# Kernel optimization log

Hardware: AMD Instinct MI355X
Metric: run time of the kernel (lower is better)

Reference implementation:

```python
import jax, jax.numpy as jnp
import numpy as np

N, E, B = 50000, 500000, 32
FEAT, HID, EDGE_DIM = 64, 128, 16
NUM_TASKS, TED, NCLS, TASKS_PER = 5000, 64, 3, 8
NLAYERS = 2


def setup_inputs() -> dict:
    key = jax.random.key(0)
    ks = jax.random.split(key, 20)
    s = 0.05
    inp = {
        "h": jax.random.normal(ks[0], (N, FEAT), jnp.float32),
        "x": jax.random.normal(ks[1], (N, 3), jnp.float32),
        "edge_index": jax.random.randint(ks[2], (2, E), 0, N, dtype=jnp.int32),
        "edge_attr": jax.random.normal(ks[3], (E, EDGE_DIM), jnp.float32),
        "batch": (jnp.arange(N, dtype=jnp.int32) * B // N).astype(jnp.int32),
        "tasks_indices": jnp.stack([
            jnp.repeat(jnp.arange(B, dtype=jnp.int32), TASKS_PER),
            jax.random.randint(ks[4], (B * TASKS_PER,), 0, NUM_TASKS, dtype=jnp.int32),
        ], axis=1),
        "batch_size": B,
        "embed_W": jax.random.normal(ks[5], (FEAT, HID), jnp.float32) * s,
        "embed_b": jnp.zeros((HID,), jnp.float32),
        "res_W": jax.random.normal(ks[6], (NLAYERS, HID, HID), jnp.float32) * s,
        "msg_W": jax.random.normal(ks[7], (NLAYERS, 2 * HID + 1, HID), jnp.float32) * s,
        "msg_b": jnp.zeros((NLAYERS, HID), jnp.float32),
        "upd_W": jax.random.normal(ks[8], (NLAYERS, 2 * HID, HID), jnp.float32) * s,
        "upd_b": jnp.zeros((NLAYERS, HID), jnp.float32),
        "mlp_W0": jax.random.normal(ks[9], (HID + TED, HID), jnp.float32) * s,
        "mlp_b0": jnp.zeros((HID,), jnp.float32),
        "mlp_W1": jax.random.normal(ks[10], (HID, HID), jnp.float32) * s,
        "mlp_b1": jnp.zeros((HID,), jnp.float32),
        "mlp_W2": jax.random.normal(ks[11], (HID, HID), jnp.float32) * s,
        "mlp_b2": jnp.zeros((HID,), jnp.float32),
        "mlp_W3": jax.random.normal(ks[12], (HID, NCLS), jnp.float32) * s,
        "mlp_b3": jnp.zeros((NCLS,), jnp.float32),
        "task_emb": jax.random.normal(ks[13], (NUM_TASKS, TED), jnp.float32),
    }
    return inp


def reference(h, x, edge_index, edge_attr, batch, tasks_indices, batch_size,
              embed_W, embed_b, res_W, msg_W, msg_b, upd_W, upd_b,
              mlp_W0, mlp_b0, mlp_W1, mlp_b1, mlp_W2, mlp_b2, mlp_W3, mlp_b3,
              task_emb):
    n = h.shape[0]
    row, col = edge_index[0], edge_index[1]
    # squared distances, identical across MP layers (positions never updated)
    dist = jnp.sum((x[row] - x[col]) ** 2, axis=1, keepdims=True)  # [E,1]
    emb = h @ embed_W + embed_b  # [N,HID]
    for l in range(NLAYERS):
        msg_in = jnp.concatenate([emb[row], emb[col], dist], axis=-1)  # [E,2H+1]
        msg = jax.nn.relu(msg_in @ msg_W[l] + msg_b[l])                # [E,H]
        aggr = jax.ops.segment_sum(msg, col, num_segments=n)           # [N,H]
        upd = jax.nn.relu(jnp.concatenate([emb, aggr], axis=-1) @ upd_W[l] + upd_b[l])
        emb = emb @ res_W[l] + upd
    # global mean pool per graph
    counts = jax.ops.segment_sum(jnp.ones((n,), emb.dtype), batch, num_segments=batch_size)
    pooled = jax.ops.segment_sum(emb, batch, num_segments=batch_size) / jnp.maximum(counts, 1.0)[:, None]
    # per-(protein, task) head; rows ordered as in the original dict-over-batch loop
    proto = tasks_indices[:, 0]
    tid = tasks_indices[:, 1]
    feat = jnp.concatenate([pooled[proto], task_emb[tid]], axis=-1)  # [K, H+TED]
    z = jax.nn.relu(feat @ mlp_W0 + mlp_b0)
    z = jax.nn.relu(z @ mlp_W1 + mlp_b1)
    z = jax.nn.relu(z @ mlp_W2 + mlp_b2)
    return z @ mlp_W3 + mlp_b3  # [K, NCLS]
```

## Files before the change

### kernel.cpp

```cpp
#include <hip/hip_runtime.h>

constexpr int NN = 50000;
constexpr int NE = 500000;
constexpr int NB = 32;
constexpr int NTROWS = 256;
constexpr int SCB = 196;
constexpr int NBLK64 = (NN + 63) / 64;

typedef __attribute__((ext_vector_type(8))) short bf16x8;
typedef __attribute__((ext_vector_type(4))) float f32x4;

static __device__ __forceinline__ unsigned short f2bf(float f) {
  unsigned u = __float_as_uint(f);
  unsigned r = (u + 0x7FFFu + ((u >> 16) & 1u)) >> 16;
  return (unsigned short)r;
}
static __device__ __forceinline__ float bf2f(unsigned short s) {
  return __uint_as_float(((unsigned)s) << 16);
}

__global__ void k_wprep(const float* __restrict__ msgW, const float* __restrict__ updW,
                        const float* __restrict__ resW, const float* __restrict__ embW,
                        unsigned short* __restrict__ wbf, int* __restrict__ cnt) {
  int idx = blockIdx.x * 256 + threadIdx.x;
  if (idx < NN) cnt[idx] = 0;
  if (idx >= 10 * 16384 + 8192) return;
  if (idx < 10 * 16384) {
    int m = idx >> 14, e = idx & 16383;
    int nn = e >> 7, kk = e & 127;
    int l = m / 5, t = m % 5;
    const float* src;
    if (t == 0)      src = msgW + (size_t)l * 257 * 128;
    else if (t == 1) src = msgW + (size_t)l * 257 * 128 + 128 * 128;
    else if (t == 2) src = updW + (size_t)l * 256 * 128;
    else if (t == 3) src = updW + (size_t)l * 256 * 128 + 128 * 128;
    else             src = resW + (size_t)l * 128 * 128;
    wbf[idx] = f2bf(src[kk * 128 + nn]);
  } else {
    int e = idx - 10 * 16384;
    int nn = e >> 6, kk = e & 63;
    wbf[idx] = f2bf(embW[kk * 128 + nn]);
  }
}

__global__ void k_count_gstart(const int* __restrict__ col, int* __restrict__ cnt,
                               const int* __restrict__ batch, int* __restrict__ gstart) {
  int e = blockIdx.x * 256 + threadIdx.x;
  if (e < NE) atomicAdd(&cnt[col[e]], 1);
  if (e < NN) {
    int b = batch[e];
    if (e == 0) gstart[b] = 0;
    else if (batch[e - 1] != b) gstart[b] = e;
    if (e == NN - 1) gstart[b + 1] = NN;
  }
}

__global__ __launch_bounds__(256) void k_scan1(const int* __restrict__ cnt,
                                               int* __restrict__ starts,
                                               int* __restrict__ bsum) {
  __shared__ int s[256];
  int t = threadIdx.x;
  int i = blockIdx.x * 256 + t;
  int v = (i < NN) ? cnt[i] : 0;
  s[t] = v; __syncthreads();
  for (int off = 1; off < 256; off <<= 1) {
    int u = (t >= off) ? s[t - off] : 0;
    __syncthreads();
    s[t] += u;
    __syncthreads();
  }
  if (i < NN) starts[i] = s[t] - v;
  if (t == 255) bsum[blockIdx.x] = s[255];
}

__global__ __launch_bounds__(256) void k_scan2(int* __restrict__ bsum) {
  __shared__ int s[256];
  int t = threadIdx.x;
  int v = (t < SCB) ? bsum[t] : 0;
  s[t] = v; __syncthreads();
  for (int off = 1; off < 256; off <<= 1) {
    int u = (t >= off) ? s[t - off] : 0;
    __syncthreads();
    s[t] += u;
    __syncthreads();
  }
  if (t < SCB) bsum[t] = s[t] - v;
}

__global__ __launch_bounds__(256) void k_scan3(int* __restrict__ starts,
                                               const int* __restrict__ bsum,
                                               int* __restrict__ cursor) {
  int i = blockIdx.x * 256 + threadIdx.x;
  if (i < NN) {
    int v = starts[i] + bsum[blockIdx.x];
    starts[i] = v;
    cursor[i] = v;
  }
  if (i == 0) starts[NN] = NE;
}

__global__ void k_scatter(const int* __restrict__ row, const int* __restrict__ col,
                          const float* __restrict__ x,
                          int* __restrict__ cursor, int2* __restrict__ spack) {
  int e = blockIdx.x * blockDim.x + threadIdx.x;
  if (e >= NE) return;
  int r = row[e], c = col[e];
  float dx = x[3*r+0] - x[3*c+0];
  float dy = x[3*r+1] - x[3*c+1];
  float dz = x[3*r+2] - x[3*c+2];
  float d = dx*dx + dy*dy + dz*dz;
  int pos = atomicAdd(&cursor[c], 1);
  spack[pos] = make_int2(r, __float_as_int(d));
}

template<int TPB>
static __device__ __forceinline__ void stage_tile64(
    unsigned short* lds, const unsigned short* __restrict__ src, int row0, int n, int tid) {
  #pragma unroll
  for (int ch = tid; ch < 1024; ch += TPB) {
    int r = ch >> 4, kc = ch & 15;
    bf16x8 v = {0,0,0,0,0,0,0,0};
    if (row0 + r < n) v = *(const bf16x8*)(src + (size_t)(row0 + r) * 128 + kc * 8);
    int byte = (r * 256 + kc * 16) ^ ((r & 7) << 4);
    *(bf16x8*)((char*)lds + byte) = v;
  }
}

template<int TPB>
static __device__ __forceinline__ void vstore_tile64(
    unsigned short* __restrict__ dst, const unsigned short* lds, int row0, int n, int tid) {
  #pragma unroll
  for (int ch = tid; ch < 1024; ch += TPB) {
    int r = ch >> 4, kc = ch & 15;
    if (row0 + r < n) {
      bf16x8 v = *(const bf16x8*)((const char*)lds + ((r * 256 + kc * 16) ^ ((r & 7) << 4)));
      *(bf16x8*)(dst + (size_t)(row0 + r) * 128 + kc * 8) = v;
    }
  }
}

static __device__ __forceinline__ void epi_to_lds64(
    unsigned short* lds, const f32x4 (&acc)[4], int lane, int c0) {
  int ccol = lane & 15, crow4 = (lane >> 4) * 4;
  int cc = c0 + ccol;
  #pragma unroll
  for (int rt = 0; rt < 4; ++rt)
    #pragma unroll
    for (int j = 0; j < 4; ++j) {
      int lrow = rt * 16 + crow4 + j;
      int lbyte = (lrow * 256 + cc * 2) ^ ((lrow & 7) << 4);
      *(unsigned short*)((char*)lds + lbyte) = f2bf(acc[rt][j]);
    }
}

__global__ __launch_bounds__(512) void k_embed_dual(
    const float* __restrict__ h, const unsigned short* __restrict__ embWt,
    const float* __restrict__ embB,
    const unsigned short* __restrict__ W1t, const unsigned short* __restrict__ W2t,
    unsigned short* __restrict__ emb, unsigned short* __restrict__ Y1,
    unsigned short* __restrict__ Y2, int n) {
  __shared__ unsigned short Hs[64 * 64];
  __shared__ unsigned short Xs[64 * 128];
  __shared__ unsigned short Y1s[64 * 128];
  __shared__ unsigned short Y2s[64 * 128];
  int row0 = blockIdx.x * 64;
  int tid = threadIdx.x;
  int wave = tid >> 6, lane = tid & 63;
  int c0 = wave * 16;
  int arow = lane & 15, kb = (lane >> 4) * 8;
  {
    int r = tid >> 3, kc = tid & 7;
    union { bf16x8 v; unsigned short s[8]; } u;
    if (row0 + r < n) {
      const float* p = h + (size_t)(row0 + r) * 64 + kc * 8;
      float4 f0 = *(const float4*)p, f1 = *(const float4*)(p + 4);
      u.s[0]=f2bf(f0.x); u.s[1]=f2bf(f0.y); u.s[2]=f2bf(f0.z); u.s[3]=f2bf(f0.w);
      u.s[4]=f2bf(f1.x); u.s[5]=f2bf(f1.y); u.s[6]=f2bf(f1.z); u.s[7]=f2bf(f1.w);
    } else {
      #pragma unroll
      for (int j = 0; j < 8; ++j) u.s[j] = 0;
    }
    int byte = (r * 128 + kc * 16) ^ ((r & 7) << 4);
    *(bf16x8*)((char*)Hs + byte) = u.v;
  }
  float bB = embB[c0 + (lane & 15)];
  __syncthreads();
  f32x4 accE[4] = {};
  #pragma unroll
  for (int ks = 0; ks < 2; ++ks) {
    bf16x8 b = *(const bf16x8*)(embWt + (size_t)(c0 + arow) * 64 + ks * 32 + kb);
    #pragma unroll
    for (int rt = 0; rt < 4; ++rt) {
      int r = rt * 16 + arow;
      int byte = (r * 128 + (ks * 32 + kb) * 2) ^ ((r & 7) << 4);
      bf16x8 a = *(const bf16x8*)((const char*)Hs + byte);
      accE[rt] = __builtin_amdgcn_mfma_f32_16x16x32_bf16(a, b, accE[rt], 0, 0, 0);
    }
  }
  {
    int ccol = lane & 15, crow4 = (lane >> 4) * 4;
    int cc = c0 + ccol;
    #pragma unroll
    for (int rt = 0; rt < 4; ++rt)
      #pragma unroll
      for (int j = 0; j < 4; ++j) {
        int lrow = rt * 16 + crow4 + j;
        int lbyte = (lrow * 256 + cc * 2) ^ ((lrow & 7) << 4);
        *(unsigned short*)((char*)Xs + lbyte) = f2bf(accE[rt][j] + bB);
      }
  }
  __syncthreads();
  f32x4 acc1[4] = {};
  f32x4 acc2[4] = {};
  #pragma unroll
  for (int ks = 0; ks < 4; ++ks) {
    int k0 = ks * 32;
    bf16x8 b1 = *(const bf16x8*)(W1t + (size_t)(c0 + arow) * 128 + k0 + kb);
    bf16x8 b2 = *(const bf16x8*)(W2t + (size_t)(c0 + arow) * 128 + k0 + kb);
    #pragma unroll
    for (int rt = 0; rt < 4; ++rt) {
      int r = rt * 16 + arow;
      int byte = (r * 256 + (k0 + kb) * 2) ^ ((r & 7) << 4);
      bf16x8 a = *(const bf16x8*)((const char*)Xs + byte);
      acc1[rt] = __builtin_amdgcn_mfma_f32_16x16x32_bf16(a, b1, acc1[rt], 0, 0, 0);
      acc2[rt] = __builtin_amdgcn_mfma_f32_16x16x32_bf16(a, b2, acc2[rt], 0, 0, 0);
    }
  }
  vstore_tile64<512>(emb, Xs, row0, n, tid);
  epi_to_lds64(Y1s, acc1, lane, c0);
  epi_to_lds64(Y2s, acc2, lane, c0);
  __syncthreads();
  vstore_tile64<512>(Y1, Y1s, row0, n, tid);
  vstore_tile64<512>(Y2, Y2s, row0, n, tid);
}

__global__ __launch_bounds__(512) void k_node_dual(
    const unsigned short* __restrict__ emb, const unsigned short* __restrict__ aggr,
    const unsigned short* __restrict__ U1t, const unsigned short* __restrict__ U2t,
    const unsigned short* __restrict__ Rt, const float* __restrict__ updb,
    const unsigned short* __restrict__ W1t, const unsigned short* __restrict__ W2t,
    unsigned short* __restrict__ out, unsigned short* __restrict__ Y1,
    unsigned short* __restrict__ Y2, int n) {
  __shared__ unsigned short Es[64 * 128];
  __shared__ unsigned short As[64 * 128];
  __shared__ unsigned short Xs[64 * 128];
  int row0 = blockIdx.x * 64;
  int tid = threadIdx.x;
  int wave = tid >> 6, lane = tid & 63;
  int c0 = wave * 16;
  int arow = lane & 15, kb = (lane >> 4) * 8;
  stage_tile64<512>(Es, emb,  row0, n, tid);
  stage_tile64<512>(As, aggr, row0, n, tid);
  float uB = updb[c0 + (lane & 15)];
  __syncthreads();
  f32x4 accU[4] = {};
  f32x4 accR[4] = {};
  #pragma unroll
  for (int ks = 0; ks < 4; ++ks) {
    int k0 = ks * 32;
    bf16x8 bU1 = *(const bf16x8*)(U1t + (size_t)(c0 + arow) * 128 + k0 + kb);
    bf16x8 bU2 = *(const bf16x8*)(U2t + (size_t)(c0 + arow) * 128 + k0 + kb);
    bf16x8 bR  = *(const bf16x8*)(Rt  + (size_t)(c0 + arow) * 128 + k0 + kb);
    #pragma unroll
    for (int rt = 0; rt < 4; ++rt) {
      int r = rt * 16 + arow;
      int byte = (r * 256 + (k0 + kb) * 2) ^ ((r & 7) << 4);
      bf16x8 aE = *(const bf16x8*)((const char*)Es + byte);
      bf16x8 aA = *(const bf16x8*)((const char*)As + byte);
      accU[rt] = __builtin_amdgcn_mfma_f32_16x16x32_bf16(aE, bU1, accU[rt], 0, 0, 0);
      accU[rt] = __builtin_amdgcn_mfma_f32_16x16x32_bf16(aA, bU2, accU[rt], 0, 0, 0);
      accR[rt] = __builtin_amdgcn_mfma_f32_16x16x32_bf16(aE, bR,  accR[rt], 0, 0, 0);
    }
  }
  {
    int ccol = lane & 15, crow4 = (lane >> 4) * 4;
    int cc = c0 + ccol;
    #pragma unroll
    for (int rt = 0; rt < 4; ++rt)
      #pragma unroll
      for (int j = 0; j < 4; ++j) {
        int lrow = rt * 16 + crow4 + j;
        int lbyte = (lrow * 256 + cc * 2) ^ ((lrow & 7) << 4);
        *(unsigned short*)((char*)Xs + lbyte) =
            f2bf(accR[rt][j] + fmaxf(accU[rt][j] + uB, 0.f));
      }
  }
  __syncthreads();
  f32x4 acc1[4] = {};
  f32x4 acc2[4] = {};
  #pragma unroll
  for (int ks = 0; ks < 4; ++ks) {
    int k0 = ks * 32;
    bf16x8 b1 = *(const bf16x8*)(W1t + (size_t)(c0 + arow) * 128 + k0 + kb);
    bf16x8 b2 = *(const bf16x8*)(W2t + (size_t)(c0 + arow) * 128 + k0 + kb);
    #pragma unroll
    for (int rt = 0; rt < 4; ++rt) {
      int r = rt * 16 + arow;
      int byte = (r * 256 + (k0 + kb) * 2) ^ ((r & 7) << 4);
      bf16x8 a = *(const bf16x8*)((const char*)Xs + byte);
      acc1[rt] = __builtin_amdgcn_mfma_f32_16x16x32_bf16(a, b1, acc1[rt], 0, 0, 0);
      acc2[rt] = __builtin_amdgcn_mfma_f32_16x16x32_bf16(a, b2, acc2[rt], 0, 0, 0);
    }
  }
  vstore_tile64<512>(out, Xs, row0, n, tid);
  epi_to_lds64(Es, acc1, lane, c0);
  epi_to_lds64(As, acc2, lane, c0);
  __syncthreads();
  vstore_tile64<512>(Y1, Es, row0, n, tid);
  vstore_tile64<512>(Y2, As, row0, n, tid);
}

__global__ __launch_bounds__(512) void k_node_pool(
    const unsigned short* __restrict__ emb, const unsigned short* __restrict__ aggr,
    const unsigned short* __restrict__ U1t, const unsigned short* __restrict__ U2t,
    const unsigned short* __restrict__ Rt, const float* __restrict__ updb,
    const int* __restrict__ batch,
    float* __restrict__ ppart, int* __restrict__ pgid, int n) {
  __shared__ unsigned short Es[64 * 128];
  __shared__ unsigned short As[64 * 128];
  __shared__ int sbat[64];
  int row0 = blockIdx.x * 64;
  int tid = threadIdx.x;
  int wave = tid >> 6, lane = tid & 63;
  int c0 = wave * 16;
  int arow = lane & 15, kb = (lane >> 4) * 8;
  stage_tile64<512>(Es, emb,  row0, n, tid);
  stage_tile64<512>(As, aggr, row0, n, tid);
  if (tid < 64) sbat[tid] = batch[min(row0 + tid, n - 1)];
  float uB = updb[c0 + (lane & 15)];
  __syncthreads();
  f32x4 accU[4] = {};
  f32x4 accR[4] = {};
  #pragma unroll
  for (int ks = 0; ks < 4; ++ks) {
    int k0 = ks * 32;
    bf16x8 bU1 = *(const bf16x8*)(U1t + (size_t)(c0 + arow) * 128 + k0 + kb);
    bf16x8 bU2 = *(const bf16x8*)(U2t + (size_t)(c0 + arow) * 128 + k0 + kb);
    bf16x8 bR  = *(const bf16x8*)(Rt  + (size_t)(c0 + arow) * 128 + k0 + kb);
    #pragma unroll
    for (int rt = 0; rt < 4; ++rt) {
      int r = rt * 16 + arow;
      int byte = (r * 256 + (k0 + kb) * 2) ^ ((r & 7) << 4);
      bf16x8 aE = *(const bf16x8*)((const char*)Es + byte);
      bf16x8 aA = *(const bf16x8*)((const char*)As + byte);
      accU[rt] = __builtin_amdgcn_mfma_f32_16x16x32_bf16(aE, bU1, accU[rt], 0, 0, 0);
      accU[rt] = __builtin_amdgcn_mfma_f32_16x16x32_bf16(aA, bU2, accU[rt], 0, 0, 0);
      accR[rt] = __builtin_amdgcn_mfma_f32_16x16x32_bf16(aE, bR,  accR[rt], 0, 0, 0);
    }
  }
  int g0 = sbat[0];
  int crow4 = (lane >> 4) * 4;
  float s0 = 0.f, s1 = 0.f;
  #pragma unroll
  for (int rt = 0; rt < 4; ++rt)
    #pragma unroll
    for (int j = 0; j < 4; ++j) {
      int lrow = rt * 16 + crow4 + j;
      if (row0 + lrow < n) {
        float v = accR[rt][j] + fmaxf(accU[rt][j] + uB, 0.f);
        if (sbat[lrow] == g0) s0 += v; else s1 += v;
      }
    }
  s0 += __shfl_xor(s0, 16); s0 += __shfl_xor(s0, 32);
  s1 += __shfl_xor(s1, 16); s1 += __shfl_xor(s1, 32);
  if ((lane >> 4) == 0) {
    int cc = c0 + (lane & 15);
    ppart[(size_t)(2 * blockIdx.x) * 128 + cc] = s0;
    ppart[(size_t)(2 * blockIdx.x + 1) * 128 + cc] = s1;
  }
  if (tid == 0) {
    int gl = sbat[63];
    pgid[2 * blockIdx.x] = g0;
    pgid[2 * blockIdx.x + 1] = (gl != g0) ? gl : -1;
  }
}

__global__ __launch_bounds__(256) void k_aggr_pull(
    const int* __restrict__ starts, const int2* __restrict__ spack,
    const unsigned short* __restrict__ A, const unsigned short* __restrict__ Bm,
    const float* __restrict__ wd, const float* __restrict__ mb,
    unsigned short* __restrict__ aggr) {
  int t = blockIdx.x * 256 + threadIdx.x;
  int node = t >> 4;
  if (node >= NN) return;
  int c0 = (t & 15) * 8;
  union { bf16x8 v; unsigned short s[8]; } ub;
  ub.v = *(const bf16x8*)(Bm + (size_t)node * 128 + c0);
  float4 w0 = *(const float4*)(wd + c0), w1 = *(const float4*)(wd + c0 + 4);
  float4 bb0 = *(const float4*)(mb + c0), bb1 = *(const float4*)(mb + c0 + 4);
  float wv[8]   = {w0.x, w0.y, w0.z, w0.w, w1.x, w1.y, w1.z, w1.w};
  float bv[8]   = {bb0.x, bb0.y, bb0.z, bb0.w, bb1.x, bb1.y, bb1.z, bb1.w};
  float basev[8], accv[8];
  #pragma unroll
  for (int j = 0; j < 8; ++j) { basev[j] = bf2f(ub.s[j]) + bv[j]; accv[j] = 0.f; }
  int s = starts[node], e = starts[node + 1];
  int i = s;
  for (; i + 4 <= e; i += 4) {
    int2 p0 = spack[i + 0], p1 = spack[i + 1];
    int2 p2 = spack[i + 2], p3 = spack[i + 3];
    union { bf16x8 v; unsigned short s[8]; } a0, a1, a2, a3;
    a0.v = *(const bf16x8*)(A + (size_t)p0.x * 128 + c0);
    a1.v = *(const bf16x8*)(A + (size_t)p1.x * 128 + c0);
    a2.v = *(const bf16x8*)(A + (size_t)p2.x * 128 + c0);
    a3.v = *(const bf16x8*)(A + (size_t)p3.x * 128 + c0);
    float d0 = __int_as_float(p0.y), d1 = __int_as_float(p1.y);
    float d2 = __int_as_float(p2.y), d3 = __int_as_float(p3.y);
    #pragma unroll
    for (int j = 0; j < 8; ++j) {
      accv[j] += fmaxf(bf2f(a0.s[j]) + fmaf(d0, wv[j], basev[j]), 0.f);
      accv[j] += fmaxf(bf2f(a1.s[j]) + fmaf(d1, wv[j], basev[j]), 0.f);
      accv[j] += fmaxf(bf2f(a2.s[j]) + fmaf(d2, wv[j], basev[j]), 0.f);
      accv[j] += fmaxf(bf2f(a3.s[j]) + fmaf(d3, wv[j], basev[j]), 0.f);
    }
  }
  for (; i < e; ++i) {
    int2 p = spack[i];
    union { bf16x8 v; unsigned short s[8]; } a;
    a.v = *(const bf16x8*)(A + (size_t)p.x * 128 + c0);
    float d = __int_as_float(p.y);
    #pragma unroll
    for (int j = 0; j < 8; ++j)
      accv[j] += fmaxf(bf2f(a.s[j]) + fmaf(d, wv[j], basev[j]), 0.f);
  }
  union { bf16x8 v; unsigned short s[8]; } o;
  #pragma unroll
  for (int j = 0; j < 8; ++j) o.s[j] = f2bf(accv[j]);
  *(bf16x8*)(aggr + (size_t)node * 128 + c0) = o.v;
}

__global__ __launch_bounds__(128) void k_pool2(const float* __restrict__ ppart,
                                               const int* __restrict__ pgid,
                                               const int* __restrict__ gstart,
                                               float* __restrict__ pooled) {
  int g = blockIdx.x, t = threadIdx.x;
  int blo = gstart[g] >> 6;
  int bhi = (gstart[g + 1] - 1) >> 6;
  float acc = 0.f;
  for (int b = blo; b <= bhi; ++b) {
    if (pgid[2 * b] == g)     acc += ppart[(size_t)(2 * b) * 128 + t];
    if (pgid[2 * b + 1] == g) acc += ppart[(size_t)(2 * b + 1) * 128 + t];
  }
  float cntf = (float)(gstart[g + 1] - gstart[g]);
  pooled[g * 128 + t] = acc / fmaxf(cntf, 1.f);
}

__global__ __launch_bounds__(128) void k_head(
    const float* __restrict__ pooled, const float* __restrict__ temb,
    const int* __restrict__ tasks,
    const float* __restrict__ W0, const float* __restrict__ b0,
    const float* __restrict__ W1, const float* __restrict__ b1,
    const float* __restrict__ W2, const float* __restrict__ b2,
    const float* __restrict__ W3, const float* __restrict__ b3,
    float* __restrict__ out) {
  __shared__ float f[192];
  __shared__ float za[128];
  __shared__ float zb[128];
  int rowi = blockIdx.x, t = threadIdx.x;
  int proto = tasks[rowi*2 + 0];
  int tid2  = tasks[rowi*2 + 1];
  f[t] = pooled[proto*128 + t];
  if (t < 64) f[128 + t] = temb[(size_t)tid2*64 + t];
  __syncthreads();
  float a = b0[t];
  for (int k = 0; k < 192; ++k) a += f[k] * W0[k*128 + t];
  za[t] = fmaxf(a, 0.f);
  __syncthreads();
  a = b1[t];
  for (int k = 0; k < 128; ++k) a += za[k] * W1[k*128 + t];
  zb[t] = fmaxf(a, 0.f);
  __syncthreads();
  a = b2[t];
  for (int k = 0; k < 128; ++k) a += zb[k] * W2[k*128 + t];
  za[t] = fmaxf(a, 0.f);
  __syncthreads();
  if (t < 3) {
    a = b3[t];
    for (int k = 0; k < 128; ++k) a += za[k] * W3[k*3 + t];
    out[rowi*3 + t] = a;
  }
}

extern "C" void kernel_launch(void* const* d_in, const int* in_sizes, int n_in,
                              void* d_out, int out_size, void* d_ws, size_t ws_size,
                              hipStream_t stream) {
  const float* h    = (const float*)d_in[0];
  const float* x    = (const float*)d_in[1];
  const int*   ei   = (const int*)d_in[2];
  const int*   batch= (const int*)d_in[4];
  const int*   tasks= (const int*)d_in[5];
  const float* embW = (const float*)d_in[7];
  const float* embB = (const float*)d_in[8];
  const float* resW = (const float*)d_in[9];
  const float* msgW = (const float*)d_in[10];
  const float* msgB = (const float*)d_in[11];
  const float* updW = (const float*)d_in[12];
  const float* updB = (const float*)d_in[13];
  const float* W0 = (const float*)d_in[14]; const float* b0 = (const float*)d_in[15];
  const float* W1 = (const float*)d_in[16]; const float* b1 = (const float*)d_in[17];
  const float* W2 = (const float*)d_in[18]; const float* b2 = (const float*)d_in[19];
  const float* W3 = (const float*)d_in[20]; const float* b3 = (const float*)d_in[21];
  const float* temb = (const float*)d_in[22];
  const int* row = ei;
  const int* col = ei + NE;

  unsigned short* bws = (unsigned short*)d_ws;
  unsigned short* e0   = bws;  bws += (size_t)NN*128;
  unsigned short* e1   = bws;  bws += (size_t)NN*128;
  unsigned short* Abuf = bws;  bws += (size_t)NN*128;
  unsigned short* Bbuf = bws;  bws += (size_t)NN*128;
  unsigned short* wbf  = bws;  bws += 10*16384 + 8192;
  float* ws = (float*)bws;
  float* pooled= ws;  ws += NB*128;
  float* ppart = ws;  ws += (size_t)2*NBLK64*128;
  int2*  spack = (int2*)ws;
  int*   iws   = (int*)(spack + NE);
  int*   cnt    = iws;  iws += NN;
  int*   starts = iws;  iws += NN + 1;
  int*   cursor = iws;  iws += NN;
  int*   gstart = iws;  iws += NB + 1;
  int*   bsum   = iws;  iws += 256;
  int*   pgid   = iws;  iws += 2*NBLK64;

  const unsigned short* embWt = wbf + (size_t)10*16384;

  k_wprep<<<672, 256, 0, stream>>>(msgW, updW, resW, embW, wbf, cnt);

  k_count_gstart<<<(NE + 255)/256, 256, 0, stream>>>(col, cnt, batch, gstart);
  k_scan1<<<SCB, 256, 0, stream>>>(cnt, starts, bsum);
  k_scan2<<<1, 256, 0, stream>>>(bsum);
  k_scan3<<<SCB, 256, 0, stream>>>(starts, bsum, cursor);
  k_scatter<<<(NE + 255)/256, 256, 0, stream>>>(row, col, x, cursor, spack);

  const unsigned short* m0W1t = wbf + (size_t)0 * 16384;
  const unsigned short* m0W2t = wbf + (size_t)1 * 16384;
  const unsigned short* u0W1t = wbf + (size_t)2 * 16384;
  const unsigned short* u0W2t = wbf + (size_t)3 * 16384;
  const unsigned short* r0Wt  = wbf + (size_t)4 * 16384;
  const unsigned short* m1W1t = wbf + (size_t)5 * 16384;
  const unsigned short* m1W2t = wbf + (size_t)6 * 16384;
  const unsigned short* u1W1t = wbf + (size_t)7 * 16384;
  const unsigned short* u1W2t = wbf + (size_t)8 * 16384;
  const unsigned short* r1Wt  = wbf + (size_t)9 * 16384;

  k_embed_dual<<<NBLK64, 512, 0, stream>>>(h, embWt, embB, m0W1t, m0W2t,
                                           e0, Abuf, Bbuf, NN);
  k_aggr_pull<<<(NN*16 + 255)/256, 256, 0, stream>>>(starts, spack, Abuf, Bbuf,
                                                     msgW + 256*128, msgB, e1);
  k_node_dual<<<NBLK64, 512, 0, stream>>>(e0, e1, u0W1t, u0W2t, r0Wt, updB,
                                          m1W1t, m1W2t, e1, Abuf, Bbuf, NN);
  k_aggr_pull<<<(NN*16 + 255)/256, 256, 0, stream>>>(starts, spack, Abuf, Bbuf,
                                                     msgW + (size_t)257*128 + 256*128,
                                                     msgB + 128, e0);
  k_node_pool<<<NBLK64, 512, 0, stream>>>(e1, e0, u1W1t, u1W2t, r1Wt, updB + 128,
                                          batch, ppart, pgid, NN);
  k_pool2<<<NB, 128, 0, stream>>>(ppart, pgid, gstart, pooled);
  k_head<<<NTROWS, 128, 0, stream>>>(pooled, temb, tasks,
                                     W0, b0, W1, b1, W2, b2, W3, b3, (float*)d_out);
}
```

Before: 213.6 us.

## Fuse edge-message pull aggregation into node update kernels via LDS staging

The separate k_aggr_pull kernels are removed. Each node-update block now gathers and aggregates the incoming-edge messages for its own 64 nodes straight into shared memory before the MFMA update. This saves two launches and the write and read-back of the aggregate buffer. Because the next layer's A/B buffers are written while other blocks still read the current ones, A/B are double-buffered, which adds workspace. The trade-off is that the gather now runs inside 512-thread, LDS-heavy blocks with fewer nodes in flight, which may hide the irregular gather latency less well than the standalone kernel did.

```diff
diff --git a/kernel.cpp b/kernel.cpp
--- a/kernel.cpp
+++ b/kernel.cpp
@@ -151,6 +151,67 @@
       int lbyte = (lrow * 256 + cc * 2) ^ ((lrow & 7) << 4);
       *(unsigned short*)((char*)lds + lbyte) = f2bf(acc[rt][j]);
     }
+}
+
+static __device__ __forceinline__ void gather_aggr_lds(
+    unsigned short* As, const int* __restrict__ starts, const int2* __restrict__ spack,
+    const unsigned short* __restrict__ A, const unsigned short* __restrict__ Bm,
+    const float* __restrict__ wd, const float* __restrict__ mb,
+    int row0, int n, int tid) {
+  int c0 = (tid & 15) * 8;
+  float4 w0 = *(const float4*)(wd + c0), w1 = *(const float4*)(wd + c0 + 4);
+  float4 bb0 = *(const float4*)(mb + c0), bb1 = *(const float4*)(mb + c0 + 4);
+  float wv[8] = {w0.x, w0.y, w0.z, w0.w, w1.x, w1.y, w1.z, w1.w};
+  float bv[8] = {bb0.x, bb0.y, bb0.z, bb0.w, bb1.x, bb1.y, bb1.z, bb1.w};
+  #pragma unroll
+  for (int pass = 0; pass < 2; ++pass) {
+    int lr = (tid >> 4) + pass * 32;
+    int node = row0 + lr;
+    union { bf16x8 v; unsigned short s[8]; } o;
+    if (node < n) {
+      union { bf16x8 v; unsigned short s[8]; } ub;
+      ub.v = *(const bf16x8*)(Bm + (size_t)node * 128 + c0);
+      float basev[8], accv[8];
+      #pragma unroll
+      for (int j = 0; j < 8; ++j) { basev[j] = bf2f(ub.s[j]) + bv[j]; accv[j] = 0.f; }
+      int s = starts[node], e = starts[node + 1];
+      int i = s;
+      for (; i + 4 <= e; i += 4) {
+        int2 p0 = spack[i + 0], p1 = spack[i + 1];
+        int2 p2 = spack[i + 2], p3 = spack[i + 3];
+        union { bf16x8 v; unsigned short s[8]; } a0, a1, a2, a3;
+        a0.v = *(const bf16x8*)(A + (size_t)p0.x * 128 + c0);
+        a1.v = *(const bf16x8*)(A + (size_t)p1.x * 128 + c0);
+        a2.v = *(const bf16x8*)(A + (size_t)p2.x * 128 + c0);
+        a3.v = *(const bf16x8*)(A + (size_t)p3.x * 128 + c0);
+        float d0 = __int_as_float(p0.y), d1 = __int_as_float(p1.y);
+        float d2 = __int_as_float(p2.y), d3 = __int_as_float(p3.y);
+        #pragma unroll
+        for (int j = 0; j < 8; ++j) {
+          accv[j] += fmaxf(bf2f(a0.s[j]) + fmaf(d0, wv[j], basev[j]), 0.f);
+          accv[j] += fmaxf(bf2f(a1.s[j]) + fmaf(d1, wv[j], basev[j]), 0.f);
+          accv[j] += fmaxf(bf2f(a2.s[j]) + fmaf(d2, wv[j], basev[j]), 0.f);
+          accv[j] += fmaxf(bf2f(a3.s[j]) + fmaf(d3, wv[j], basev[j]), 0.f);
+        }
+      }
+      for (; i < e; ++i) {
+        int2 p = spack[i];
+        union { bf16x8 v; unsigned short s[8]; } a;
+        a.v = *(const bf16x8*)(A + (size_t)p.x * 128 + c0);
+        float d = __int_as_float(p.y);
+        #pragma unroll
+        for (int j = 0; j < 8; ++j)
+          accv[j] += fmaxf(bf2f(a.s[j]) + fmaf(d, wv[j], basev[j]), 0.f);
+      }
+      #pragma unroll
+      for (int j = 0; j < 8; ++j) o.s[j] = f2bf(accv[j]);
+    } else {
+      #pragma unroll
+      for (int j = 0; j < 8; ++j) o.s[j] = 0;
+    }
+    int byte = (lr * 256 + (tid & 15) * 16) ^ ((lr & 7) << 4);
+    *(bf16x8*)((char*)As + byte) = o.v;
+  }
 }
 
 __global__ __launch_bounds__(512) void k_embed_dual(
@@ -234,8 +295,11 @@
   vstore_tile64<512>(Y2, Y2s, row0, n, tid);
 }
 
-__global__ __launch_bounds__(512) void k_node_dual(
-    const unsigned short* __restrict__ emb, const unsigned short* __restrict__ aggr,
+__global__ __launch_bounds__(512) void k_node_dual_pull(
+    const unsigned short* __restrict__ emb,
+    const int* __restrict__ starts, const int2* __restrict__ spack,
+    const unsigned short* __restrict__ Agth, const unsigned short* __restrict__ Bm,
+    const float* __restrict__ wd, const float* __restrict__ mb,
     const unsigned short* __restrict__ U1t, const unsigned short* __restrict__ U2t,
     const unsigned short* __restrict__ Rt, const float* __restrict__ updb,
     const unsigned short* __restrict__ W1t, const unsigned short* __restrict__ W2t,
@@ -249,8 +313,8 @@
   int wave = tid >> 6, lane = tid & 63;
   int c0 = wave * 16;
   int arow = lane & 15, kb = (lane >> 4) * 8;
-  stage_tile64<512>(Es, emb,  row0, n, tid);
-  stage_tile64<512>(As, aggr, row0, n, tid);
+  stage_tile64<512>(Es, emb, row0, n, tid);
+  gather_aggr_lds(As, starts, spack, Agth, Bm, wd, mb, row0, n, tid);
   float uB = updb[c0 + (lane & 15)];
   __syncthreads();
   f32x4 accU[4] = {};
@@ -310,8 +374,11 @@
   vstore_tile64<512>(Y2, As, row0, n, tid);
 }
 
-__global__ __launch_bounds__(512) void k_node_pool(
-    const unsigned short* __restrict__ emb, const unsigned short* __restrict__ aggr,
+__global__ __launch_bounds__(512) void k_node_pool_pull(
+    const unsigned short* __restrict__ emb,
+    const int* __restrict__ starts, const int2* __restrict__ spack,
+    const unsigned short* __restrict__ Agth, const unsigned short* __restrict__ Bm,
+    const float* __restrict__ wd, const float* __restrict__ mb,
     const unsigned short* __restrict__ U1t, const unsigned short* __restrict__ U2t,
     const unsigned short* __restrict__ Rt, const float* __restrict__ updb,
     const int* __restrict__ batch,
@@ -324,9 +391,9 @@
   int wave = tid >> 6, lane = tid & 63;
   int c0 = wave * 16;
   int arow = lane & 15, kb = (lane >> 4) * 8;
-  stage_tile64<512>(Es, emb,  row0, n, tid);
-  stage_tile64<512>(As, aggr, row0, n, tid);
+  stage_tile64<512>(Es, emb, row0, n, tid);
   if (tid < 64) sbat[tid] = batch[min(row0 + tid, n - 1)];
+  gather_aggr_lds(As, starts, spack, Agth, Bm, wd, mb, row0, n, tid);
   float uB = updb[c0 + (lane & 15)];
   __syncthreads();
   f32x4 accU[4] = {};
@@ -373,59 +440,6 @@
     pgid[2 * blockIdx.x] = g0;
     pgid[2 * blockIdx.x + 1] = (gl != g0) ? gl : -1;
   }
-}
-
-__global__ __launch_bounds__(256) void k_aggr_pull(
-    const int* __restrict__ starts, const int2* __restrict__ spack,
-    const unsigned short* __restrict__ A, const unsigned short* __restrict__ Bm,
-    const float* __restrict__ wd, const float* __restrict__ mb,
-    unsigned short* __restrict__ aggr) {
-  int t = blockIdx.x * 256 + threadIdx.x;
-  int node = t >> 4;
-  if (node >= NN) return;
-  int c0 = (t & 15) * 8;
-  union { bf16x8 v; unsigned short s[8]; } ub;
-  ub.v = *(const bf16x8*)(Bm + (size_t)node * 128 + c0);
-  float4 w0 = *(const float4*)(wd + c0), w1 = *(const float4*)(wd + c0 + 4);
-  float4 bb0 = *(const float4*)(mb + c0), bb1 = *(const float4*)(mb + c0 + 4);
-  float wv[8]   = {w0.x, w0.y, w0.z, w0.w, w1.x, w1.y, w1.z, w1.w};
-  float bv[8]   = {bb0.x, bb0.y, bb0.z, bb0.w, bb1.x, bb1.y, bb1.z, bb1.w};
-  float basev[8], accv[8];
-  #pragma unroll
-  for (int j = 0; j < 8; ++j) { basev[j] = bf2f(ub.s[j]) + bv[j]; accv[j] = 0.f; }
-  int s = starts[node], e = starts[node + 1];
-  int i = s;
-  for (; i + 4 <= e; i += 4) {
-    int2 p0 = spack[i + 0], p1 = spack[i + 1];
-    int2 p2 = spack[i + 2], p3 = spack[i + 3];
-    union { bf16x8 v; unsigned short s[8]; } a0, a1, a2, a3;
-    a0.v = *(const bf16x8*)(A + (size_t)p0.x * 128 + c0);
-    a1.v = *(const bf16x8*)(A + (size_t)p1.x * 128 + c0);
-    a2.v = *(const bf16x8*)(A + (size_t)p2.x * 128 + c0);
-    a3.v = *(const bf16x8*)(A + (size_t)p3.x * 128 + c0);
-    float d0 = __int_as_float(p0.y), d1 = __int_as_float(p1.y);
-    float d2 = __int_as_float(p2.y), d3 = __int_as_float(p3.y);
-    #pragma unroll
-    for (int j = 0; j < 8; ++j) {
-      accv[j] += fmaxf(bf2f(a0.s[j]) + fmaf(d0, wv[j], basev[j]), 0.f);
-      accv[j] += fmaxf(bf2f(a1.s[j]) + fmaf(d1, wv[j], basev[j]), 0.f);
-      accv[j] += fmaxf(bf2f(a2.s[j]) + fmaf(d2, wv[j], basev[j]), 0.f);
-      accv[j] += fmaxf(bf2f(a3.s[j]) + fmaf(d3, wv[j], basev[j]), 0.f);
-    }
-  }
-  for (; i < e; ++i) {
-    int2 p = spack[i];
-    union { bf16x8 v; unsigned short s[8]; } a;
-    a.v = *(const bf16x8*)(A + (size_t)p.x * 128 + c0);
-    float d = __int_as_float(p.y);
-    #pragma unroll
-    for (int j = 0; j < 8; ++j)
-      accv[j] += fmaxf(bf2f(a.s[j]) + fmaf(d, wv[j], basev[j]), 0.f);
-  }
-  union { bf16x8 v; unsigned short s[8]; } o;
-  #pragma unroll
-  for (int j = 0; j < 8; ++j) o.s[j] = f2bf(accv[j]);
-  *(bf16x8*)(aggr + (size_t)node * 128 + c0) = o.v;
 }
 
 __global__ __launch_bounds__(128) void k_pool2(const float* __restrict__ ppart,
@@ -506,8 +520,10 @@
   unsigned short* bws = (unsigned short*)d_ws;
   unsigned short* e0   = bws;  bws += (size_t)NN*128;
   unsigned short* e1   = bws;  bws += (size_t)NN*128;
-  unsigned short* Abuf = bws;  bws += (size_t)NN*128;
-  unsigned short* Bbuf = bws;  bws += (size_t)NN*128;
+  unsigned short* A0   = bws;  bws += (size_t)NN*128;
+  unsigned short* B0   = bws;  bws += (size_t)NN*128;
+  unsigned short* A1   = bws;  bws += (size_t)NN*128;
+  unsigned short* B1   = bws;  bws += (size_t)NN*128;
   unsigned short* wbf  = bws;  bws += 10*16384 + 8192;
   float* ws = (float*)bws;
   float* pooled= ws;  ws += NB*128;
@@ -543,16 +559,16 @@
   const unsigned short* r1Wt  = wbf + (size_t)9 * 16384;
 
   k_embed_dual<<<NBLK64, 512, 0, stream>>>(h, embWt, embB, m0W1t, m0W2t,
-                                           e0, Abuf, Bbuf, NN);
-  k_aggr_pull<<<(NN*16 + 255)/256, 256, 0, stream>>>(starts, spack, Abuf, Bbuf,
-                                                     msgW + 256*128, msgB, e1);
-  k_node_dual<<<NBLK64, 512, 0, stream>>>(e0, e1, u0W1t, u0W2t, r0Wt, updB,
-                                          m1W1t, m1W2t, e1, Abuf, Bbuf, NN);
-  k_aggr_pull<<<(NN*16 + 255)/256, 256, 0, stream>>>(starts, spack, Abuf, Bbuf,
-                                                     msgW + (size_t)257*128 + 256*128,
-                                                     msgB + 128, e0);
-  k_node_pool<<<NBLK64, 512, 0, stream>>>(e1, e0, u1W1t, u1W2t, r1Wt, updB + 128,
-                                          batch, ppart, pgid, NN);
+                                           e0, A0, B0, NN);
+  k_node_dual_pull<<<NBLK64, 512, 0, stream>>>(e0, starts, spack, A0, B0,
+                                               msgW + 256*128, msgB,
+                                               u0W1t, u0W2t, r0Wt, updB,
+                                               m1W1t, m1W2t, e1, A1, B1, NN);
+  k_node_pool_pull<<<NBLK64, 512, 0, stream>>>(e1, starts, spack, A1, B1,
+                                               msgW + (size_t)257*128 + 256*128,
+                                               msgB + 128,
+                                               u1W1t, u1W2t, r1Wt, updB + 128,
+                                               batch, ppart, pgid, NN);
   k_pool2<<<NB, 128, 0, stream>>>(ppart, pgid, gstart, pooled);
   k_head<<<NTROWS, 128, 0, stream>>>(pooled, temb, tasks,
                                      W0, b0, W1, b1, W2, b2, W3, b3, (float*)d_out);
```

Measured after the change: 208.6 us. 1.02x faster.
